# Kernel tuning notes

Measured on AMD Instinct MI355X. Metric: run time of the kernel, lower is better.

## Reference

```python
import jax, jax.numpy as jnp
import numpy as np

N, E, C = 50000, 800000, 128
NEG_SLOPE = 0.01

def leaky(v):
    return jnp.where(v >= 0, v, NEG_SLOPE * v)

def setup_inputs() -> dict:
    key = jax.random.key(0)
    ks = jax.random.split(key, 16)
    s = lambda *sh: 1.0 / np.sqrt(sh[0])
    return {
        "x": jax.random.normal(ks[0], (N, C), dtype=jnp.float32),
        "pos": jax.random.normal(ks[1], (N, 3), dtype=jnp.float32),
        "edge_index": jax.random.randint(ks[2], (2, E), 0, N, dtype=jnp.int64),
        # mlp_h: Linear(C,C) -> LeakyReLU -> Linear(C,3) -> Tanh
        "h_w1": jax.random.uniform(ks[3], (C, C), jnp.float32, -s(C), s(C)),
        "h_b1": jax.random.uniform(ks[4], (C,), jnp.float32, -s(C), s(C)),
        "h_w2": jax.random.uniform(ks[5], (C, 3), jnp.float32, -s(C), s(C)),
        "h_b2": jax.random.uniform(ks[6], (3,), jnp.float32, -s(C), s(C)),
        # mlp_f: Linear(C+3, C) -> LeakyReLU
        "f_w": jax.random.uniform(ks[7], (C + 3, C), jnp.float32, -s(C + 3), s(C + 3)),
        "f_b": jax.random.uniform(ks[8], (C,), jnp.float32, -s(C + 3), s(C + 3)),
        # mlp_g: Linear(C,C) -> LeakyReLU -> Linear(C,C)
        "g_w1": jax.random.uniform(ks[9], (C, C), jnp.float32, -s(C), s(C)),
        "g_b1": jax.random.uniform(ks[10], (C,), jnp.float32, -s(C), s(C)),
        "g_w2": jax.random.uniform(ks[11], (C, C), jnp.float32, -s(C), s(C)),
        "g_b2": jax.random.uniform(ks[12], (C,), jnp.float32, -s(C), s(C)),
    }

def reference(x, pos, edge_index, h_w1, h_b1, h_w2, h_b2, f_w, f_b,
              g_w1, g_b1, g_w2, g_b2):
    src = edge_index[0]  # j (source)
    dst = edge_index[1]  # i (target)
    # delta_i = mlp_h(x_i): [N, 3]
    delta = jnp.tanh(leaky(x @ h_w1 + h_b1) @ h_w2 + h_b2)
    # edge message: mlp_f(cat([pos_j - pos_i + delta_i, x_j]))  -> [E, C]
    rel = pos[src] - pos[dst] + delta[dst]            # [E, 3]
    msg_in = jnp.concatenate([rel, x[src]], axis=-1)  # [E, C+3]
    e = leaky(msg_in @ f_w + f_b)                     # [E, C]
    # sum-aggregate messages at target nodes
    aggr = jax.ops.segment_sum(e, dst, num_segments=N)  # [N, C]
    # out = mlp_g(aggr) + x
    out = leaky(aggr @ g_w1 + g_b1) @ g_w2 + g_b2 + x
    return out
```

## Files before the change

kernel.cpp:

```cpp
#include <hip/hip_runtime.h>
#include <hip/hip_bf16.h>
#include <math.h>


typedef __attribute__((ext_vector_type(8))) short bf16x8;
typedef __attribute__((ext_vector_type(4))) float f32x4;

#define LEAKY(v) ((v) >= 0.0f ? (v) : 0.01f * (v))

#define KMAX 512
#define S3_BATCH 8192

static __device__ __forceinline__ unsigned short f2bf(float f) {
    unsigned u = __float_as_uint(f);
    u = (u + 0x7fffu + ((u >> 16) & 1u)) >> 16;
    return (unsigned short)u;
}

union ABu { unsigned short u[8]; bf16x8 v; };

static __device__ __forceinline__ bf16x8 cvt8(const float* __restrict__ p) {
    ABu r;
    const float4 v0 = *(const float4*)p;
    const float4 v1 = *(const float4*)(p + 4);
    r.u[0] = f2bf(v0.x); r.u[1] = f2bf(v0.y); r.u[2] = f2bf(v0.z); r.u[3] = f2bf(v0.w);
    r.u[4] = f2bf(v1.x); r.u[5] = f2bf(v1.y); r.u[6] = f2bf(v1.z); r.u[7] = f2bf(v1.w);
    return r.v;
}

static __device__ __forceinline__ bf16x8 zero_ab() {
    ABu r;
    #pragma unroll
    for (int i = 0; i < 8; ++i) r.u[i] = 0;
    return r.v;
}

static __device__ __forceinline__ void stage_weight(
    const unsigned short* __restrict__ src, unsigned short (*dst)[136], int tid)
{
    #pragma unroll
    for (int it = 0; it < 8; ++it) {
        const int c   = it * 256 + tid;
        const int row = c >> 4;
        const int col = (c & 15) * 8;
        *(uint4*)&dst[row][col] = *(const uint4*)(src + row * 128 + col);
    }
}

__global__ __launch_bounds__(128) void prep_weights(
    const float* __restrict__ h_w1, const float* __restrict__ f_w,
    const float* __restrict__ g_w1, const float* __restrict__ g_w2,
    unsigned short* __restrict__ Wht, unsigned short* __restrict__ Wft,
    unsigned short* __restrict__ G1t, unsigned short* __restrict__ G2t,
    int* __restrict__ bincnt, int* __restrict__ done)
{
    const int j = blockIdx.x;
    const int k = threadIdx.x;
    if (j == 0) {
        for (int i = k; i < KMAX; i += 128) bincnt[i] = 0;
        if (k == 0) *done = 0;
    }
    Wht[j * 128 + k] = f2bf(h_w1[(size_t)k * 128 + j]);
    Wft[j * 128 + k] = f2bf(f_w[(size_t)(3 + k) * 128 + j]);
    G1t[j * 128 + k] = f2bf(g_w1[(size_t)k * 128 + j]);
    G2t[j * 128 + k] = f2bf(g_w2[(size_t)k * 128 + j]);
}

__global__ __launch_bounds__(256) void node_pre(
    const float* __restrict__ x, const float* __restrict__ pos,
    const unsigned short* __restrict__ Wht, const float* __restrict__ h_b1,
    const float* __restrict__ h_w2, const float* __restrict__ h_b2,
    const unsigned short* __restrict__ Wft, const float* __restrict__ f_b,
    const float* __restrict__ fw3,
    float* __restrict__ deltap, unsigned short* __restrict__ Zb, int N)
{
    __shared__ unsigned short Ws[128][136];
    __shared__ float cb[128][8];

    const int tid  = threadIdx.x;
    const int lane = tid & 63;
    const int wave = tid >> 6;
    const int quad = lane >> 4;
    const int l16  = lane & 15;
    const int row0 = blockIdx.x * 64 + wave * 16;

    if (tid < 128) {
        cb[tid][0] = h_b1[tid];
        cb[tid][1] = f_b[tid];
        cb[tid][2] = h_w2[tid * 3 + 0];
        cb[tid][3] = h_w2[tid * 3 + 1];
        cb[tid][4] = h_w2[tid * 3 + 2];
        cb[tid][5] = fw3[tid];
        cb[tid][6] = fw3[128 + tid];
        cb[tid][7] = fw3[256 + tid];
    }
    stage_weight(Wht, Ws, tid);

    bf16x8 a[4];
    {
        const int row = row0 + l16;
        if (row < N) {
            const float* xp = x + (size_t)row * 128 + quad * 8;
            #pragma unroll
            for (int kc = 0; kc < 4; ++kc) a[kc] = cvt8(xp + kc * 32);
        } else {
            #pragma unroll
            for (int kc = 0; kc < 4; ++kc) a[kc] = zero_ab();
        }
    }

    float px[4], py[4], pz[4];
    #pragma unroll
    for (int reg = 0; reg < 4; ++reg) {
        const int grow = row0 + quad * 4 + reg;
        const int gr = (grow < N) ? grow : 0;
        px[reg] = pos[(size_t)gr * 3 + 0];
        py[reg] = pos[(size_t)gr * 3 + 1];
        pz[reg] = pos[(size_t)gr * 3 + 2];
    }
    __syncthreads();

    f32x4 acch[8];
    #pragma unroll
    for (int nt = 0; nt < 8; ++nt) acch[nt] = (f32x4){0.f, 0.f, 0.f, 0.f};
    #pragma unroll
    for (int nt = 0; nt < 8; ++nt) {
        const unsigned short* wp = &Ws[nt * 16 + l16][quad * 8];
        #pragma unroll
        for (int kc = 0; kc < 4; ++kc) {
            const bf16x8 b = *(const bf16x8*)(wp + kc * 32);
            acch[nt] = __builtin_amdgcn_mfma_f32_16x16x32_bf16(a[kc], b, acch[nt], 0, 0, 0);
        }
    }

    __syncthreads();
    stage_weight(Wft, Ws, tid);
    __syncthreads();

    f32x4 accf[8];
    #pragma unroll
    for (int nt = 0; nt < 8; ++nt) accf[nt] = (f32x4){0.f, 0.f, 0.f, 0.f};
    #pragma unroll
    for (int nt = 0; nt < 8; ++nt) {
        const unsigned short* wp = &Ws[nt * 16 + l16][quad * 8];
        #pragma unroll
        for (int kc = 0; kc < 4; ++kc) {
            const bf16x8 b = *(const bf16x8*)(wp + kc * 32);
            accf[nt] = __builtin_amdgcn_mfma_f32_16x16x32_bf16(a[kc], b, accf[nt], 0, 0, 0);
        }
    }

    float p[4][3];
    #pragma unroll
    for (int r = 0; r < 4; ++r) { p[r][0] = 0.f; p[r][1] = 0.f; p[r][2] = 0.f; }

    #pragma unroll
    for (int nt = 0; nt < 8; ++nt) {
        const int col = nt * 16 + l16;
        const float b1  = cb[col][0];
        const float fb  = cb[col][1];
        const float w20 = cb[col][2];
        const float w21 = cb[col][3];
        const float w22 = cb[col][4];
        const float wxc = cb[col][5];
        const float wyc = cb[col][6];
        const float wzc = cb[col][7];
        #pragma unroll
        for (int reg = 0; reg < 4; ++reg) {
            const int grow = row0 + quad * 4 + reg;
            float h = acch[nt][reg] + b1;
            h = LEAKY(h);
            p[reg][0] += h * w20;
            p[reg][1] += h * w21;
            p[reg][2] += h * w22;
            if (grow < N) {
                const float z = accf[nt][reg] + fb
                              + px[reg] * wxc + py[reg] * wyc + pz[reg] * wzc;
                Zb[(size_t)grow * 128 + col] = f2bf(z);
            }
        }
    }

    #pragma unroll
    for (int reg = 0; reg < 4; ++reg)
        #pragma unroll
        for (int c = 0; c < 3; ++c) {
            float v = p[reg][c];
            v += __shfl_down(v, 8);
            v += __shfl_down(v, 4);
            v += __shfl_down(v, 2);
            v += __shfl_down(v, 1);
            p[reg][c] = v;
        }

    if (l16 == 0) {
        #pragma unroll
        for (int reg = 0; reg < 4; ++reg) {
            const int grow = row0 + quad * 4 + reg;
            if (grow < N) {
                deltap[(size_t)grow * 3 + 0] = tanhf(p[reg][0] + h_b2[0]) - px[reg];
                deltap[(size_t)grow * 3 + 1] = tanhf(p[reg][1] + h_b2[1]) - py[reg];
                deltap[(size_t)grow * 3 + 2] = tanhf(p[reg][2] + h_b2[2]) - pz[reg];
            }
        }
    }
}

__global__ __launch_bounds__(512) void coarse_hist(
    const int* __restrict__ ei, int* __restrict__ bincnt,
    int* __restrict__ binstart, int* __restrict__ cursors,
    int* __restrict__ done, int E, int K)
{
    __shared__ int h[KMAX];
    __shared__ int s[512];
    __shared__ int lastflag;
    const int tid = threadIdx.x;
    for (int k = tid; k < K; k += 512) h[k] = 0;
    __syncthreads();
    const int stride = gridDim.x * 512;
    for (int e = blockIdx.x * 512 + tid; e < E; e += stride)
        atomicAdd(&h[ei[(size_t)E + e] >> 7], 1);
    __syncthreads();
    for (int k = tid; k < K; k += 512) {
        const int v = h[k];
        if (v) atomicAdd(&bincnt[k], v);
    }
    __threadfence();
    __syncthreads();
    if (tid == 0) lastflag = (atomicAdd(done, 1) == (int)gridDim.x - 1) ? 1 : 0;
    __syncthreads();
    if (!lastflag) return;

    const int c = (tid < K) ? atomicAdd(&bincnt[tid], 0) : 0;
    s[tid] = c;
    __syncthreads();
    for (int d = 1; d < 512; d <<= 1) {
        const int t = (tid >= d) ? s[tid - d] : 0;
        __syncthreads();
        s[tid] += t;
        __syncthreads();
    }
    if (tid < K) {
        binstart[tid] = s[tid] - c;
        cursors[tid]  = s[tid] - c;
    }
    if (tid == 0) binstart[K] = E;
}

__global__ __launch_bounds__(1024) void binsort(
    const int* __restrict__ ei, int* __restrict__ cursors,
    unsigned int* __restrict__ binned, int E, int K)
{
    __shared__ int h[KMAX];
    __shared__ int hE[KMAX];
    __shared__ int cur[KMAX];
    __shared__ int gbase[KMAX];
    __shared__ int s[512];
    __shared__ unsigned int stage[S3_BATCH];
    __shared__ unsigned short binid[S3_BATCH];

    const int tid = threadIdx.x;
    const int e0  = blockIdx.x * S3_BATCH;
    const int m   = min(S3_BATCH, E - e0);

    for (int k = tid; k < K; k += 1024) h[k] = 0;
    __syncthreads();

    #pragma unroll
    for (int j = 0; j < S3_BATCH / 1024; ++j) {
        const int i = j * 1024 + tid;
        if (i < m) atomicAdd(&h[ei[(size_t)E + e0 + i] >> 7], 1);
    }
    __syncthreads();

    int c = 0;
    if (tid < 512) {
        c = (tid < K) ? h[tid] : 0;
        s[tid] = c;
    }
    __syncthreads();
    for (int d = 1; d < 512; d <<= 1) {
        int t = 0;
        if (tid < 512 && tid >= d) t = s[tid - d];
        __syncthreads();
        if (tid < 512) s[tid] += t;
        __syncthreads();
    }
    if (tid < K) {
        const int ex = s[tid] - c;
        hE[tid]  = ex;
        cur[tid] = ex;
        gbase[tid] = c ? atomicAdd(&cursors[tid], c) : 0;
    }
    __syncthreads();

    #pragma unroll
    for (int j = 0; j < S3_BATCH / 1024; ++j) {
        const int i = j * 1024 + tid;
        if (i < m) {
            const int src = ei[e0 + i];
            const int dst = ei[(size_t)E + e0 + i];
            const int k = dst >> 7;
            const int p = atomicAdd(&cur[k], 1);
            stage[p] = (unsigned int)src | ((unsigned int)(dst & 127) << 16);
            binid[p] = (unsigned short)k;
        }
    }
    __syncthreads();

    #pragma unroll
    for (int j = 0; j < S3_BATCH / 1024; ++j) {
        const int i = j * 1024 + tid;
        if (i < m) {
            const int k = binid[i];
            binned[(size_t)gbase[k] + (i - hE[k])] = stage[i];
        }
    }
}

__global__ __launch_bounds__(256) void bin_finalize(
    const unsigned int* __restrict__ binned, const int* __restrict__ binstart,
    unsigned short* __restrict__ srcs_sorted,
    int* __restrict__ counts, int* __restrict__ offs_end, int N)
{
    __shared__ int h[128];
    __shared__ int s[128];
    __shared__ int cur[128];
    const int tid = threadIdx.x;
    const int b   = blockIdx.x;
    const int s0  = binstart[b];
    const int s1  = binstart[b + 1];
    const int len = s1 - s0;

    if (tid < 128) h[tid] = 0;
    __syncthreads();

    for (int i = tid; i < len; i += 256)
        atomicAdd(&h[binned[(size_t)s0 + i] >> 16], 1);
    __syncthreads();

    if (tid < 128) s[tid] = h[tid];
    __syncthreads();
    for (int d = 1; d < 128; d <<= 1) {
        int t = 0;
        if (tid < 128 && tid >= d) t = s[tid - d];
        __syncthreads();
        if (tid < 128) s[tid] += t;
        __syncthreads();
    }

    if (tid < 128) {
        const int dglob = b * 128 + tid;
        if (dglob < N) {
            counts[dglob]   = h[tid];
            offs_end[dglob] = s0 + s[tid];
        }
        cur[tid] = s0 + s[tid] - h[tid];
    }
    __syncthreads();

    for (int i = tid; i < len; i += 256) {
        const unsigned int r = binned[(size_t)s0 + i];
        const int p = atomicAdd(&cur[r >> 16], 1);
        srcs_sorted[p] = (unsigned short)(r & 0xffffu);
    }
}

__global__ __launch_bounds__(256) void aggregate_kernel(
    const unsigned short* __restrict__ srcs_sorted,
    const int* __restrict__ offs_end,
    const int* __restrict__ counts,
    const float* __restrict__ deltap,
    const unsigned short* __restrict__ Zb,
    const float* __restrict__ fw3,
    unsigned short* __restrict__ Ab,
    int N)
{
    const int lane = threadIdx.x & 63;
    const int d = blockIdx.x * 4 + (threadIdx.x >> 6);
    if (d >= N) return;

    const int quarter = lane >> 4;
    const int cl      = (lane & 15) * 8;

    const float q0 = deltap[(size_t)d * 3 + 0];
    const float q1 = deltap[(size_t)d * 3 + 1];
    const float q2 = deltap[(size_t)d * 3 + 2];

    float qd[8];
    #pragma unroll
    for (int j = 0; j < 8; ++j)
        qd[j] = q0 * fw3[cl + j] + q1 * fw3[128 + cl + j] + q2 * fw3[256 + cl + j];

    const int len   = counts[d];
    const int start = offs_end[d] - len;

    float acc[8] = {0.f, 0.f, 0.f, 0.f, 0.f, 0.f, 0.f, 0.f};

    for (int chunk = 0; chunk < len; chunk += 64) {
        const int m = min(64, len - chunk);
        int idx = 0;
        if (lane < m) idx = srcs_sorted[start + chunk + lane];

        int t = 0;
        #pragma unroll 4
        for (; t + 4 <= m; t += 4) {
            const int s = __shfl(idx, t + quarter);
            const uint4 y = *(const uint4*)(Zb + (size_t)s * 128 + cl);
            const float f0 = __uint_as_float((y.x & 0xffffu) << 16);
            const float f1 = __uint_as_float(y.x & 0xffff0000u);
            const float f2 = __uint_as_float((y.y & 0xffffu) << 16);
            const float f3 = __uint_as_float(y.y & 0xffff0000u);
            const float f4 = __uint_as_float((y.z & 0xffffu) << 16);
            const float f5 = __uint_as_float(y.z & 0xffff0000u);
            const float f6 = __uint_as_float((y.w & 0xffffu) << 16);
            const float f7 = __uint_as_float(y.w & 0xffff0000u);
            const float z0 = f0 + qd[0], z1 = f1 + qd[1];
            const float z2 = f2 + qd[2], z3 = f3 + qd[3];
            const float z4 = f4 + qd[4], z5 = f5 + qd[5];
            const float z6 = f6 + qd[6], z7 = f7 + qd[7];
            acc[0] += fmaxf(z0, 0.01f * z0);
            acc[1] += fmaxf(z1, 0.01f * z1);
            acc[2] += fmaxf(z2, 0.01f * z2);
            acc[3] += fmaxf(z3, 0.01f * z3);
            acc[4] += fmaxf(z4, 0.01f * z4);
            acc[5] += fmaxf(z5, 0.01f * z5);
            acc[6] += fmaxf(z6, 0.01f * z6);
            acc[7] += fmaxf(z7, 0.01f * z7);
        }
        if (t < m) {
            const int e = t + quarter;
            const int s = __shfl(idx, e);
            if (e < m) {
                const uint4 y = *(const uint4*)(Zb + (size_t)s * 128 + cl);
                const float f0 = __uint_as_float((y.x & 0xffffu) << 16);
                const float f1 = __uint_as_float(y.x & 0xffff0000u);
                const float f2 = __uint_as_float((y.y & 0xffffu) << 16);
                const float f3 = __uint_as_float(y.y & 0xffff0000u);
                const float f4 = __uint_as_float((y.z & 0xffffu) << 16);
                const float f5 = __uint_as_float(y.z & 0xffff0000u);
                const float f6 = __uint_as_float((y.w & 0xffffu) << 16);
                const float f7 = __uint_as_float(y.w & 0xffff0000u);
                const float z0 = f0 + qd[0], z1 = f1 + qd[1];
                const float z2 = f2 + qd[2], z3 = f3 + qd[3];
                const float z4 = f4 + qd[4], z5 = f5 + qd[5];
                const float z6 = f6 + qd[6], z7 = f7 + qd[7];
                acc[0] += fmaxf(z0, 0.01f * z0);
                acc[1] += fmaxf(z1, 0.01f * z1);
                acc[2] += fmaxf(z2, 0.01f * z2);
                acc[3] += fmaxf(z3, 0.01f * z3);
                acc[4] += fmaxf(z4, 0.01f * z4);
                acc[5] += fmaxf(z5, 0.01f * z5);
                acc[6] += fmaxf(z6, 0.01f * z6);
                acc[7] += fmaxf(z7, 0.01f * z7);
            }
        }
    }

    #pragma unroll
    for (int j = 0; j < 8; ++j) {
        acc[j] += __shfl_xor(acc[j], 16);
        acc[j] += __shfl_xor(acc[j], 32);
    }
    if (quarter == 0) {
        ABu o;
        #pragma unroll
        for (int j = 0; j < 8; ++j) o.u[j] = f2bf(acc[j]);
        *(bf16x8*)(Ab + (size_t)d * 128 + cl) = o.v;
    }
}

__global__ __launch_bounds__(256) void gemm_g(
    const unsigned short* __restrict__ Ab,
    const unsigned short* __restrict__ G1t, const float* __restrict__ g_b1,
    const unsigned short* __restrict__ G2t, const float* __restrict__ g_b2,
    const float* __restrict__ x,
    float* __restrict__ out, int N)
{
    __shared__ unsigned short Ws[128][136];
    __shared__ unsigned short Ts[64][136];

    const int tid  = threadIdx.x;
    const int lane = tid & 63;
    const int wave = tid >> 6;
    const int quad = lane >> 4;
    const int l16  = lane & 15;
    const int row0 = blockIdx.x * 64 + wave * 16;

    stage_weight(G1t, Ws, tid);

    bf16x8 a[4];
    {
        const int row = row0 + l16;
        if (row < N) {
            const unsigned short* ap = Ab + (size_t)row * 128 + quad * 8;
            #pragma unroll
            for (int kc = 0; kc < 4; ++kc) a[kc] = *(const bf16x8*)(ap + kc * 32);
        } else {
            #pragma unroll
            for (int kc = 0; kc < 4; ++kc) a[kc] = zero_ab();
        }
    }
    __syncthreads();

    f32x4 acc[8];
    #pragma unroll
    for (int nt = 0; nt < 8; ++nt) acc[nt] = (f32x4){0.f, 0.f, 0.f, 0.f};
    #pragma unroll
    for (int nt = 0; nt < 8; ++nt) {
        const unsigned short* wp = &Ws[nt * 16 + l16][quad * 8];
        #pragma unroll
        for (int kc = 0; kc < 4; ++kc) {
            const bf16x8 b = *(const bf16x8*)(wp + kc * 32);
            acc[nt] = __builtin_amdgcn_mfma_f32_16x16x32_bf16(a[kc], b, acc[nt], 0, 0, 0);
        }
    }

    #pragma unroll
    for (int nt = 0; nt < 8; ++nt) {
        const int col = nt * 16 + l16;
        const float b1 = g_b1[col];
        #pragma unroll
        for (int reg = 0; reg < 4; ++reg) {
            float t = acc[nt][reg] + b1;
            t = LEAKY(t);
            Ts[wave * 16 + quad * 4 + reg][col] = f2bf(t);
        }
    }
    __syncthreads();
    stage_weight(G2t, Ws, tid);
    __syncthreads();

    bf16x8 a2[4];
    {
        const unsigned short* tp = &Ts[wave * 16 + l16][quad * 8];
        #pragma unroll
        for (int kc = 0; kc < 4; ++kc) a2[kc] = *(const bf16x8*)(tp + kc * 32);
    }

    f32x4 acc2[8];
    #pragma unroll
    for (int nt = 0; nt < 8; ++nt) acc2[nt] = (f32x4){0.f, 0.f, 0.f, 0.f};
    #pragma unroll
    for (int nt = 0; nt < 8; ++nt) {
        const unsigned short* wp = &Ws[nt * 16 + l16][quad * 8];
        #pragma unroll
        for (int kc = 0; kc < 4; ++kc) {
            const bf16x8 b = *(const bf16x8*)(wp + kc * 32);
            acc2[nt] = __builtin_amdgcn_mfma_f32_16x16x32_bf16(a2[kc], b, acc2[nt], 0, 0, 0);
        }
    }

    #pragma unroll
    for (int nt = 0; nt < 8; ++nt) {
        const int col = nt * 16 + l16;
        const float b2 = g_b2[col];
        #pragma unroll
        for (int reg = 0; reg < 4; ++reg) {
            const int grow = row0 + quad * 4 + reg;
            if (grow < N)
                out[(size_t)grow * 128 + col] =
                    acc2[nt][reg] + b2 + x[(size_t)grow * 128 + col];
        }
    }
}

extern "C" void kernel_launch(void* const* d_in, const int* in_sizes, int n_in,
                              void* d_out, int out_size, void* d_ws, size_t ws_size,
                              hipStream_t stream) {
    const float* x    = (const float*)d_in[0];
    const float* pos  = (const float*)d_in[1];
    const int*   ei   = (const int*)d_in[2];
    const float* h_w1 = (const float*)d_in[3];
    const float* h_b1 = (const float*)d_in[4];
    const float* h_w2 = (const float*)d_in[5];
    const float* h_b2 = (const float*)d_in[6];
    const float* f_w  = (const float*)d_in[7];
    const float* f_b  = (const float*)d_in[8];
    const float* g_w1 = (const float*)d_in[9];
    const float* g_b1 = (const float*)d_in[10];
    const float* g_w2 = (const float*)d_in[11];
    const float* g_b2 = (const float*)d_in[12];
    float* out = (float*)d_out;

    const int N = in_sizes[0] / 128;
    const int E = in_sizes[2] / 2;
    const int K = (N + 127) >> 7;

    float* deltap         = (float*)d_ws;
    unsigned short* Zb    = (unsigned short*)(deltap + (size_t)N * 3);
    int* counts           = (int*)(Zb + (size_t)N * 128);
    int* offs_end         = counts + N;
    int* bincnt           = offs_end + N;
    int* binstart         = bincnt + KMAX;
    int* cursors          = binstart + (KMAX + 1);
    int* done             = cursors + KMAX;
    unsigned short* srcs  = (unsigned short*)(done + 1);
    unsigned int* binned  = (unsigned int*)(srcs + (((size_t)E + 1) & ~(size_t)1));
    unsigned short* Wht   = (unsigned short*)(binned + E);
    unsigned short* Wft   = Wht + 128 * 128;
    unsigned short* G1t   = Wft + 128 * 128;
    unsigned short* G2t   = G1t + 128 * 128;
    unsigned short* Ab    = G2t + 128 * 128;

    const int tile_blocks = (N + 63) / 64;
    const int sort_blocks = (E + S3_BATCH - 1) / S3_BATCH;

    prep_weights<<<128, 128, 0, stream>>>(h_w1, f_w, g_w1, g_w2, Wht, Wft, G1t, G2t,
                                          bincnt, done);

    coarse_hist<<<128, 512, 0, stream>>>(ei, bincnt, binstart, cursors, done, E, K);

    node_pre<<<tile_blocks, 256, 0, stream>>>(x, pos, Wht, h_b1, h_w2, h_b2, Wft, f_b,
                                              f_w, deltap, Zb, N);

    binsort<<<sort_blocks, 1024, 0, stream>>>(ei, cursors, binned, E, K);
    bin_finalize<<<K, 256, 0, stream>>>(binned, binstart, srcs, counts, offs_end, N);

    aggregate_kernel<<<(N + 3) / 4, 256, 0, stream>>>(
        srcs, offs_end, counts, deltap, Zb, f_w, Ab, N);

    gemm_g<<<tile_blocks, 256, 0, stream>>>(Ab, G1t, g_b1, G2t, g_b2, x, out, N);
}
```

Baseline: 226.5 us.

## Fuse bin finalize and aggregation into one shared-memory atomic accumulation kernel

```diff
diff --git a/kernel.cpp b/kernel.cpp
--- a/kernel.cpp
+++ b/kernel.cpp
@@ -318,155 +318,66 @@
     }
 }
 
-__global__ __launch_bounds__(256) void bin_finalize(
+__global__ __launch_bounds__(256) void bin_aggregate(
     const unsigned int* __restrict__ binned, const int* __restrict__ binstart,
-    unsigned short* __restrict__ srcs_sorted,
-    int* __restrict__ counts, int* __restrict__ offs_end, int N)
-{
-    __shared__ int h[128];
-    __shared__ int s[128];
-    __shared__ int cur[128];
-    const int tid = threadIdx.x;
-    const int b   = blockIdx.x;
-    const int s0  = binstart[b];
-    const int s1  = binstart[b + 1];
-    const int len = s1 - s0;
-
-    if (tid < 128) h[tid] = 0;
-    __syncthreads();
-
-    for (int i = tid; i < len; i += 256)
-        atomicAdd(&h[binned[(size_t)s0 + i] >> 16], 1);
-    __syncthreads();
-
-    if (tid < 128) s[tid] = h[tid];
-    __syncthreads();
-    for (int d = 1; d < 128; d <<= 1) {
-        int t = 0;
-        if (tid < 128 && tid >= d) t = s[tid - d];
-        __syncthreads();
-        if (tid < 128) s[tid] += t;
-        __syncthreads();
-    }
-
-    if (tid < 128) {
-        const int dglob = b * 128 + tid;
-        if (dglob < N) {
-            counts[dglob]   = h[tid];
-            offs_end[dglob] = s0 + s[tid];
-        }
-        cur[tid] = s0 + s[tid] - h[tid];
-    }
-    __syncthreads();
-
-    for (int i = tid; i < len; i += 256) {
-        const unsigned int r = binned[(size_t)s0 + i];
-        const int p = atomicAdd(&cur[r >> 16], 1);
-        srcs_sorted[p] = (unsigned short)(r & 0xffffu);
-    }
-}
-
-__global__ __launch_bounds__(256) void aggregate_kernel(
-    const unsigned short* __restrict__ srcs_sorted,
-    const int* __restrict__ offs_end,
-    const int* __restrict__ counts,
     const float* __restrict__ deltap,
     const unsigned short* __restrict__ Zb,
     const float* __restrict__ fw3,
     unsigned short* __restrict__ Ab,
     int N)
 {
-    const int lane = threadIdx.x & 63;
-    const int d = blockIdx.x * 4 + (threadIdx.x >> 6);
-    if (d >= N) return;
-
-    const int quarter = lane >> 4;
-    const int cl      = (lane & 15) * 8;
-
-    const float q0 = deltap[(size_t)d * 3 + 0];
-    const float q1 = deltap[(size_t)d * 3 + 1];
-    const float q2 = deltap[(size_t)d * 3 + 2];
-
-    float qd[8];
-    #pragma unroll
-    for (int j = 0; j < 8; ++j)
-        qd[j] = q0 * fw3[cl + j] + q1 * fw3[128 + cl + j] + q2 * fw3[256 + cl + j];
-
-    const int len   = counts[d];
-    const int start = offs_end[d] - len;
-
-    float acc[8] = {0.f, 0.f, 0.f, 0.f, 0.f, 0.f, 0.f, 0.f};
-
-    for (int chunk = 0; chunk < len; chunk += 64) {
-        const int m = min(64, len - chunk);
-        int idx = 0;
-        if (lane < m) idx = srcs_sorted[start + chunk + lane];
-
-        int t = 0;
-        #pragma unroll 4
-        for (; t + 4 <= m; t += 4) {
-            const int s = __shfl(idx, t + quarter);
-            const uint4 y = *(const uint4*)(Zb + (size_t)s * 128 + cl);
-            const float f0 = __uint_as_float((y.x & 0xffffu) << 16);
-            const float f1 = __uint_as_float(y.x & 0xffff0000u);
-            const float f2 = __uint_as_float((y.y & 0xffffu) << 16);
-            const float f3 = __uint_as_float(y.y & 0xffff0000u);
-            const float f4 = __uint_as_float((y.z & 0xffffu) << 16);
-            const float f5 = __uint_as_float(y.z & 0xffff0000u);
-            const float f6 = __uint_as_float((y.w & 0xffffu) << 16);
-            const float f7 = __uint_as_float(y.w & 0xffff0000u);
-            const float z0 = f0 + qd[0], z1 = f1 + qd[1];
-            const float z2 = f2 + qd[2], z3 = f3 + qd[3];
-            const float z4 = f4 + qd[4], z5 = f5 + qd[5];
-            const float z6 = f6 + qd[6], z7 = f7 + qd[7];
-            acc[0] += fmaxf(z0, 0.01f * z0);
-            acc[1] += fmaxf(z1, 0.01f * z1);
-            acc[2] += fmaxf(z2, 0.01f * z2);
-            acc[3] += fmaxf(z3, 0.01f * z3);
-            acc[4] += fmaxf(z4, 0.01f * z4);
-            acc[5] += fmaxf(z5, 0.01f * z5);
-            acc[6] += fmaxf(z6, 0.01f * z6);
-            acc[7] += fmaxf(z7, 0.01f * z7);
-        }
-        if (t < m) {
-            const int e = t + quarter;
-            const int s = __shfl(idx, e);
-            if (e < m) {
-                const uint4 y = *(const uint4*)(Zb + (size_t)s * 128 + cl);
-                const float f0 = __uint_as_float((y.x & 0xffffu) << 16);
-                const float f1 = __uint_as_float(y.x & 0xffff0000u);
-                const float f2 = __uint_as_float((y.y & 0xffffu) << 16);
-                const float f3 = __uint_as_float(y.y & 0xffff0000u);
-                const float f4 = __uint_as_float((y.z & 0xffffu) << 16);
-                const float f5 = __uint_as_float(y.z & 0xffff0000u);
-                const float f6 = __uint_as_float((y.w & 0xffffu) << 16);
-                const float f7 = __uint_as_float(y.w & 0xffff0000u);
-                const float z0 = f0 + qd[0], z1 = f1 + qd[1];
-                const float z2 = f2 + qd[2], z3 = f3 + qd[3];
-                const float z4 = f4 + qd[4], z5 = f5 + qd[5];
-                const float z6 = f6 + qd[6], z7 = f7 + qd[7];
-                acc[0] += fmaxf(z0, 0.01f * z0);
-                acc[1] += fmaxf(z1, 0.01f * z1);
-                acc[2] += fmaxf(z2, 0.01f * z2);
-                acc[3] += fmaxf(z3, 0.01f * z3);
-                acc[4] += fmaxf(z4, 0.01f * z4);
-                acc[5] += fmaxf(z5, 0.01f * z5);
-                acc[6] += fmaxf(z6, 0.01f * z6);
-                acc[7] += fmaxf(z7, 0.01f * z7);
-            }
-        }
-    }
-
-    #pragma unroll
-    for (int j = 0; j < 8; ++j) {
-        acc[j] += __shfl_xor(acc[j], 16);
-        acc[j] += __shfl_xor(acc[j], 32);
-    }
-    if (quarter == 0) {
-        ABu o;
-        #pragma unroll
-        for (int j = 0; j < 8; ++j) o.u[j] = f2bf(acc[j]);
-        *(bf16x8*)(Ab + (size_t)d * 128 + cl) = o.v;
+    __shared__ float acc[128 * 64];
+
+    const int tid  = threadIdx.x;
+    const int lane = tid & 63;
+    const int wv   = tid >> 6;
+    const int b    = blockIdx.x >> 1;
+    const int half = blockIdx.x & 1;
+    const int ch   = half * 64 + lane;
+    const int d0   = b * 128;
+
+    #pragma unroll
+    for (int i = 0; i < 8; ++i)
+        ((float4*)acc)[i * 256 + tid] = make_float4(0.f, 0.f, 0.f, 0.f);
+
+    const float fx = fw3[ch];
+    const float fy = fw3[128 + ch];
+    const float fz = fw3[256 + ch];
+
+    const int s0 = binstart[b];
+    const int s1 = binstart[b + 1];
+    __syncthreads();
+
+    #pragma unroll 4
+    for (int i = s0 + wv; i < s1; i += 4) {
+        const unsigned int r = binned[i];
+        const int dl  = r >> 16;
+        const int src = r & 0xffffu;
+        const float* dp = deltap + (size_t)(d0 + dl) * 3;
+        const float q0 = dp[0], q1 = dp[1], q2 = dp[2];
+        const unsigned short zu = Zb[(size_t)src * 128 + ch];
+        float z = __uint_as_float((unsigned)zu << 16)
+                + (q0 * fx + q1 * fy + q2 * fz);
+        z = fmaxf(z, 0.01f * z);
+        atomicAdd(&acc[dl * 64 + lane], z);
+    }
+    __syncthreads();
+
+    #pragma unroll
+    for (int i = 0; i < 8; ++i) {
+        const int flat = i * 256 + tid;
+        const int row  = flat >> 4;
+        const int c4   = (flat & 15) * 4;
+        const int dglob = d0 + row;
+        if (dglob < N) {
+            const float* ap = &acc[row * 64 + c4];
+            unsigned long long pk =
+                  (unsigned long long)f2bf(ap[0])
+                | ((unsigned long long)f2bf(ap[1]) << 16)
+                | ((unsigned long long)f2bf(ap[2]) << 32)
+                | ((unsigned long long)f2bf(ap[3]) << 48);
+            *(unsigned long long*)(Ab + (size_t)dglob * 128 + half * 64 + c4) = pk;
+        }
     }
 }
 
@@ -589,14 +500,11 @@
 
     float* deltap         = (float*)d_ws;
     unsigned short* Zb    = (unsigned short*)(deltap + (size_t)N * 3);
-    int* counts           = (int*)(Zb + (size_t)N * 128);
-    int* offs_end         = counts + N;
-    int* bincnt           = offs_end + N;
+    int* bincnt           = (int*)(Zb + (size_t)N * 128);
     int* binstart         = bincnt + KMAX;
     int* cursors          = binstart + (KMAX + 1);
     int* done             = cursors + KMAX;
-    unsigned short* srcs  = (unsigned short*)(done + 1);
-    unsigned int* binned  = (unsigned int*)(srcs + (((size_t)E + 1) & ~(size_t)1));
+    unsigned int* binned  = (unsigned int*)(done + 1);
     unsigned short* Wht   = (unsigned short*)(binned + E);
     unsigned short* Wft   = Wht + 128 * 128;
     unsigned short* G1t   = Wft + 128 * 128;
@@ -615,10 +523,8 @@
                                               f_w, deltap, Zb, N);
 
     binsort<<<sort_blocks, 1024, 0, stream>>>(ei, cursors, binned, E, K);
-    bin_finalize<<<K, 256, 0, stream>>>(binned, binstart, srcs, counts, offs_end, N);
-
-    aggregate_kernel<<<(N + 3) / 4, 256, 0, stream>>>(
-        srcs, offs_end, counts, deltap, Zb, f_w, Ab, N);
+
+    bin_aggregate<<<K * 2, 256, 0, stream>>>(binned, binstart, deltap, Zb, f_w, Ab, N);
 
     gemm_g<<<tile_blocks, 256, 0, stream>>>(Ab, G1t, g_b1, G2t, g_b2, x, out, N);
 }
```

New measurement: 860.5 us. +280.0%, slower.

## Fuse bin finalize and aggregation into one kernel with LDS source lists

Applied to the files above, without the earlier changes.

```diff
diff --git a/kernel.cpp b/kernel.cpp
--- a/kernel.cpp
+++ b/kernel.cpp
@@ -10,6 +10,7 @@
 
 #define KMAX 512
 #define S3_BATCH 8192
+#define AGG_CAP 16384
 
 static __device__ __forceinline__ unsigned short f2bf(float f) {
     unsigned u = __float_as_uint(f);
@@ -318,24 +319,31 @@
     }
 }
 
-__global__ __launch_bounds__(256) void bin_finalize(
+__global__ __launch_bounds__(1024) void bin_csr_aggregate(
     const unsigned int* __restrict__ binned, const int* __restrict__ binstart,
-    unsigned short* __restrict__ srcs_sorted,
-    int* __restrict__ counts, int* __restrict__ offs_end, int N)
+    const float* __restrict__ deltap,
+    const unsigned short* __restrict__ Zb,
+    const float* __restrict__ fw3,
+    unsigned short* __restrict__ srcs_g,
+    unsigned short* __restrict__ Ab,
+    int N)
 {
     __shared__ int h[128];
     __shared__ int s[128];
     __shared__ int cur[128];
+    __shared__ unsigned short sl[AGG_CAP];
+
     const int tid = threadIdx.x;
     const int b   = blockIdx.x;
     const int s0  = binstart[b];
     const int s1  = binstart[b + 1];
     const int len = s1 - s0;
+    const bool fits = (len <= AGG_CAP);
 
     if (tid < 128) h[tid] = 0;
     __syncthreads();
 
-    for (int i = tid; i < len; i += 256)
+    for (int i = tid; i < len; i += 1024)
         atomicAdd(&h[binned[(size_t)s0 + i] >> 16], 1);
     __syncthreads();
 
@@ -348,91 +356,54 @@
         if (tid < 128) s[tid] += t;
         __syncthreads();
     }
-
-    if (tid < 128) {
-        const int dglob = b * 128 + tid;
-        if (dglob < N) {
-            counts[dglob]   = h[tid];
-            offs_end[dglob] = s0 + s[tid];
-        }
-        cur[tid] = s0 + s[tid] - h[tid];
-    }
-    __syncthreads();
-
-    for (int i = tid; i < len; i += 256) {
+    if (tid < 128) cur[tid] = s[tid] - h[tid];
+    __syncthreads();
+
+    for (int i = tid; i < len; i += 1024) {
         const unsigned int r = binned[(size_t)s0 + i];
         const int p = atomicAdd(&cur[r >> 16], 1);
-        srcs_sorted[p] = (unsigned short)(r & 0xffffu);
-    }
-}
-
-__global__ __launch_bounds__(256) void aggregate_kernel(
-    const unsigned short* __restrict__ srcs_sorted,
-    const int* __restrict__ offs_end,
-    const int* __restrict__ counts,
-    const float* __restrict__ deltap,
-    const unsigned short* __restrict__ Zb,
-    const float* __restrict__ fw3,
-    unsigned short* __restrict__ Ab,
-    int N)
-{
-    const int lane = threadIdx.x & 63;
-    const int d = blockIdx.x * 4 + (threadIdx.x >> 6);
-    if (d >= N) return;
-
+        if (fits) sl[p] = (unsigned short)(r & 0xffffu);
+        else      srcs_g[(size_t)s0 + p] = (unsigned short)(r & 0xffffu);
+    }
+    __threadfence_block();
+    __syncthreads();
+
+    const int lane    = tid & 63;
+    const int wv      = tid >> 6;
     const int quarter = lane >> 4;
     const int cl      = (lane & 15) * 8;
-
-    const float q0 = deltap[(size_t)d * 3 + 0];
-    const float q1 = deltap[(size_t)d * 3 + 1];
-    const float q2 = deltap[(size_t)d * 3 + 2];
-
-    float qd[8];
-    #pragma unroll
-    for (int j = 0; j < 8; ++j)
-        qd[j] = q0 * fw3[cl + j] + q1 * fw3[128 + cl + j] + q2 * fw3[256 + cl + j];
-
-    const int len   = counts[d];
-    const int start = offs_end[d] - len;
-
-    float acc[8] = {0.f, 0.f, 0.f, 0.f, 0.f, 0.f, 0.f, 0.f};
-
-    for (int chunk = 0; chunk < len; chunk += 64) {
-        const int m = min(64, len - chunk);
-        int idx = 0;
-        if (lane < m) idx = srcs_sorted[start + chunk + lane];
-
-        int t = 0;
-        #pragma unroll 4
-        for (; t + 4 <= m; t += 4) {
-            const int s = __shfl(idx, t + quarter);
-            const uint4 y = *(const uint4*)(Zb + (size_t)s * 128 + cl);
-            const float f0 = __uint_as_float((y.x & 0xffffu) << 16);
-            const float f1 = __uint_as_float(y.x & 0xffff0000u);
-            const float f2 = __uint_as_float((y.y & 0xffffu) << 16);
-            const float f3 = __uint_as_float(y.y & 0xffff0000u);
-            const float f4 = __uint_as_float((y.z & 0xffffu) << 16);
-            const float f5 = __uint_as_float(y.z & 0xffff0000u);
-            const float f6 = __uint_as_float((y.w & 0xffffu) << 16);
-            const float f7 = __uint_as_float(y.w & 0xffff0000u);
-            const float z0 = f0 + qd[0], z1 = f1 + qd[1];
-            const float z2 = f2 + qd[2], z3 = f3 + qd[3];
-            const float z4 = f4 + qd[4], z5 = f5 + qd[5];
-            const float z6 = f6 + qd[6], z7 = f7 + qd[7];
-            acc[0] += fmaxf(z0, 0.01f * z0);
-            acc[1] += fmaxf(z1, 0.01f * z1);
-            acc[2] += fmaxf(z2, 0.01f * z2);
-            acc[3] += fmaxf(z3, 0.01f * z3);
-            acc[4] += fmaxf(z4, 0.01f * z4);
-            acc[5] += fmaxf(z5, 0.01f * z5);
-            acc[6] += fmaxf(z6, 0.01f * z6);
-            acc[7] += fmaxf(z7, 0.01f * z7);
-        }
-        if (t < m) {
-            const int e = t + quarter;
-            const int s = __shfl(idx, e);
-            if (e < m) {
-                const uint4 y = *(const uint4*)(Zb + (size_t)s * 128 + cl);
+    const int d0      = b * 128;
+
+    for (int dl = wv; dl < 128; dl += 16) {
+        const int d = d0 + dl;
+        if (d >= N) continue;
+
+        const int len_d = h[dl];
+        const int start = s[dl] - h[dl];
+
+        const float q0 = deltap[(size_t)d * 3 + 0];
+        const float q1 = deltap[(size_t)d * 3 + 1];
+        const float q2 = deltap[(size_t)d * 3 + 2];
+
+        float qd[8];
+        #pragma unroll
+        for (int j = 0; j < 8; ++j)
+            qd[j] = q0 * fw3[cl + j] + q1 * fw3[128 + cl + j] + q2 * fw3[256 + cl + j];
+
+        float acc[8] = {0.f, 0.f, 0.f, 0.f, 0.f, 0.f, 0.f, 0.f};
+
+        for (int chunk = 0; chunk < len_d; chunk += 64) {
+            const int m = min(64, len_d - chunk);
+            int idx = 0;
+            if (lane < m)
+                idx = fits ? (int)sl[start + chunk + lane]
+                           : (int)srcs_g[(size_t)s0 + start + chunk + lane];
+
+            int t = 0;
+            #pragma unroll 4
+            for (; t + 4 <= m; t += 4) {
+                const int sidx = __shfl(idx, t + quarter);
+                const uint4 y = *(const uint4*)(Zb + (size_t)sidx * 128 + cl);
                 const float f0 = __uint_as_float((y.x & 0xffffu) << 16);
                 const float f1 = __uint_as_float(y.x & 0xffff0000u);
                 const float f2 = __uint_as_float((y.y & 0xffffu) << 16);
@@ -454,19 +425,46 @@
                 acc[6] += fmaxf(z6, 0.01f * z6);
                 acc[7] += fmaxf(z7, 0.01f * z7);
             }
-        }
-    }
-
-    #pragma unroll
-    for (int j = 0; j < 8; ++j) {
-        acc[j] += __shfl_xor(acc[j], 16);
-        acc[j] += __shfl_xor(acc[j], 32);
-    }
-    if (quarter == 0) {
-        ABu o;
-        #pragma unroll
-        for (int j = 0; j < 8; ++j) o.u[j] = f2bf(acc[j]);
-        *(bf16x8*)(Ab + (size_t)d * 128 + cl) = o.v;
+            if (t < m) {
+                const int e = t + quarter;
+                const int sidx = __shfl(idx, e);
+                if (e < m) {
+                    const uint4 y = *(const uint4*)(Zb + (size_t)sidx * 128 + cl);
+                    const float f0 = __uint_as_float((y.x & 0xffffu) << 16);
+                    const float f1 = __uint_as_float(y.x & 0xffff0000u);
+                    const float f2 = __uint_as_float((y.y & 0xffffu) << 16);
+                    const float f3 = __uint_as_float(y.y & 0xffff0000u);
+                    const float f4 = __uint_as_float((y.z & 0xffffu) << 16);
+                    const float f5 = __uint_as_float(y.z & 0xffff0000u);
+                    const float f6 = __uint_as_float((y.w & 0xffffu) << 16);
+                    const float f7 = __uint_as_float(y.w & 0xffff0000u);
+                    const float z0 = f0 + qd[0], z1 = f1 + qd[1];
+                    const float z2 = f2 + qd[2], z3 = f3 + qd[3];
+                    const float z4 = f4 + qd[4], z5 = f5 + qd[5];
+                    const float z6 = f6 + qd[6], z7 = f7 + qd[7];
+                    acc[0] += fmaxf(z0, 0.01f * z0);
+                    acc[1] += fmaxf(z1, 0.01f * z1);
+                    acc[2] += fmaxf(z2, 0.01f * z2);
+                    acc[3] += fmaxf(z3, 0.01f * z3);
+                    acc[4] += fmaxf(z4, 0.01f * z4);
+                    acc[5] += fmaxf(z5, 0.01f * z5);
+                    acc[6] += fmaxf(z6, 0.01f * z6);
+                    acc[7] += fmaxf(z7, 0.01f * z7);
+                }
+            }
+        }
+
+        #pragma unroll
+        for (int j = 0; j < 8; ++j) {
+            acc[j] += __shfl_xor(acc[j], 16);
+            acc[j] += __shfl_xor(acc[j], 32);
+        }
+        if (quarter == 0) {
+            ABu o;
+            #pragma unroll
+            for (int j = 0; j < 8; ++j) o.u[j] = f2bf(acc[j]);
+            *(bf16x8*)(Ab + (size_t)d * 128 + cl) = o.v;
+        }
     }
 }
 
@@ -589,15 +587,13 @@
 
     float* deltap         = (float*)d_ws;
     unsigned short* Zb    = (unsigned short*)(deltap + (size_t)N * 3);
-    int* counts           = (int*)(Zb + (size_t)N * 128);
-    int* offs_end         = counts + N;
-    int* bincnt           = offs_end + N;
+    int* bincnt           = (int*)(Zb + (size_t)N * 128);
     int* binstart         = bincnt + KMAX;
     int* cursors          = binstart + (KMAX + 1);
     int* done             = cursors + KMAX;
-    unsigned short* srcs  = (unsigned short*)(done + 1);
-    unsigned int* binned  = (unsigned int*)(srcs + (((size_t)E + 1) & ~(size_t)1));
-    unsigned short* Wht   = (unsigned short*)(binned + E);
+    unsigned int* binned  = (unsigned int*)(done + 1);
+    unsigned short* srcs  = (unsigned short*)(binned + E);
+    unsigned short* Wht   = srcs + (((size_t)E + 1) & ~(size_t)1);
     unsigned short* Wft   = Wht + 128 * 128;
     unsigned short* G1t   = Wft + 128 * 128;
     unsigned short* G2t   = G1t + 128 * 128;
@@ -615,10 +611,9 @@
                                               f_w, deltap, Zb, N);
 
     binsort<<<sort_blocks, 1024, 0, stream>>>(ei, cursors, binned, E, K);
-    bin_finalize<<<K, 256, 0, stream>>>(binned, binstart, srcs, counts, offs_end, N);
-
-    aggregate_kernel<<<(N + 3) / 4, 256, 0, stream>>>(
-        srcs, offs_end, counts, deltap, Zb, f_w, Ab, N);
+
+    bin_csr_aggregate<<<K, 1024, 0, stream>>>(binned, binstart, deltap, Zb, f_w,
+                                              srcs, Ab, N);
 
     gemm_g<<<tile_blocks, 256, 0, stream>>>(Ab, G1t, g_b1, G2t, g_b2, x, out, N);
 }
```

After: 224.8 us. Within noise of the previous version (-0.7%).
